# Performance work log

Measured on AMD Instinct MI355X. Metric: run time of the kernel, lower is better.

## Reference

```python
import jax, jax.numpy as jnp
import numpy as np

BATCH, IN_WIDTH, OUT_FEATURES, FAN_IN = 512, 4096, 4096, 128

def setup_inputs() -> dict:
    key = jax.random.key(0)
    k1, k2, k3, k4 = jax.random.split(key, 4)
    input = jax.random.normal(k1, (BATCH, IN_WIDTH), dtype=jnp.float32)
    weight = jax.random.normal(k2, (OUT_FEATURES, FAN_IN), dtype=jnp.float32)
    bias = jax.random.normal(k3, (OUT_FEATURES,), dtype=jnp.float32)
    indx_seqs = jax.random.randint(k4, (OUT_FEATURES, FAN_IN), 0, IN_WIDTH, dtype=jnp.int64)
    return {"input": input, "weight": weight, "bias": bias, "indx_seqs": indx_seqs}

def reference(input, weight, bias, indx_seqs):
    # gather: (B, out_features, fan_in)
    gathered = input[:, indx_seqs]
    # elementwise mul with weight (out_features, fan_in), reduce over fan_in
    return jnp.einsum('bof,of->bo', gathered, weight) + bias
```

## Files before the change

### kernel.cpp

```cpp
#include <hip/hip_runtime.h>
#include <hip/hip_bf16.h>

#define BATCH    512
#define IN_WIDTH 4096
#define OUT_F    4096
#define FAN_IN   128

__global__ __launch_bounds__(256) void k_transpose_in(const float* __restrict__ in,
                                                      __hip_bfloat16* __restrict__ inT) {
  __shared__ float tile[32][33];
  const int jt = blockIdx.x * 32;
  const int bt = blockIdx.y * 32;
  const int tx = threadIdx.x;
  const int ty = threadIdx.y;
#pragma unroll
  for (int r = 0; r < 32; r += 8) {
    tile[ty + r][tx] = in[(size_t)(bt + ty + r) * IN_WIDTH + (jt + tx)];
  }
  __syncthreads();
#pragma unroll
  for (int r = 0; r < 32; r += 8) {
    inT[(size_t)(jt + ty + r) * BATCH + (bt + tx)] = __float2bfloat16(tile[tx][ty + r]);
  }
}

__global__ __launch_bounds__(256) void k_gather_fma(const __hip_bfloat16* __restrict__ inT,
                                                    const float* __restrict__ weight,
                                                    const float* __restrict__ bias,
                                                    const int* __restrict__ idx,
                                                    float* __restrict__ outT) {
  const int o = blockIdx.x;
  const int t = threadIdx.x;
  const int* __restrict__ idxo = idx + (size_t)o * FAN_IN;
  const float* __restrict__ wo = weight + (size_t)o * FAN_IN;
  const uint16_t* __restrict__ inTu = reinterpret_cast<const uint16_t*>(inT);

  float acc0 = 0.f, acc1 = 0.f;
#pragma unroll 8
  for (int f = 0; f < FAN_IN; ++f) {
    const int   j = idxo[f];
    const float w = wo[f];
    const uint32_t v = *reinterpret_cast<const uint32_t*>(inTu + (size_t)j * BATCH + 2 * t);
    const float lo = __uint_as_float(v << 16);
    const float hi = __uint_as_float(v & 0xffff0000u);
    acc0 = fmaf(lo, w, acc0);
    acc1 = fmaf(hi, w, acc1);
  }
  const float bz = bias[o];
  float2 r = make_float2(acc0 + bz, acc1 + bz);
  *reinterpret_cast<float2*>(outT + (size_t)o * BATCH + 2 * t) = r;
}

__global__ __launch_bounds__(256) void k_transpose_out(const float* __restrict__ outT,
                                                       float* __restrict__ out) {
  __shared__ float tile[32][33];
  const int ot = blockIdx.x * 32;
  const int bt = blockIdx.y * 32;
  const int tx = threadIdx.x;
  const int ty = threadIdx.y;
#pragma unroll
  for (int r = 0; r < 32; r += 8) {
    tile[ty + r][tx] = outT[(size_t)(ot + ty + r) * BATCH + (bt + tx)];
  }
  __syncthreads();
#pragma unroll
  for (int r = 0; r < 32; r += 8) {
    out[(size_t)(bt + ty + r) * OUT_F + (ot + tx)] = tile[tx][ty + r];
  }
}

extern "C" void kernel_launch(void* const* d_in, const int* in_sizes, int n_in,
                              void* d_out, int out_size, void* d_ws, size_t ws_size,
                              hipStream_t stream) {
  const float* input  = (const float*)d_in[0];
  const float* weight = (const float*)d_in[1];
  const float* bias   = (const float*)d_in[2];
  const int*   idx    = (const int*)d_in[3];
  float* out = (float*)d_out;

  __hip_bfloat16* inT = (__hip_bfloat16*)d_ws;
  float* outT = (float*)((char*)d_ws + (size_t)IN_WIDTH * BATCH * sizeof(__hip_bfloat16));

  dim3 tblk(32, 8);
  k_transpose_in<<<dim3(IN_WIDTH / 32, BATCH / 32), tblk, 0, stream>>>(input, inT);
  k_gather_fma<<<dim3(OUT_F), dim3(256), 0, stream>>>(inT, weight, bias, idx, outT);
  k_transpose_out<<<dim3(OUT_F / 32, BATCH / 32), tblk, 0, stream>>>(outT, out);
}
```

Baseline: 43.21 us.

## Split transposed input into batch halves and map one wave per output feature

The transposed bf16 input is stored as two batch halves of 256 columns each. The gather kernel now assigns one 64-lane wave per output feature and handles one batch half per block-y, with each lane loading 8 bytes (4 bf16 values) instead of 4. Because the feature index is wave-uniform, the idx and weight loads can become scalar loads, and each gathered row is a 512-byte contiguous chunk. The cost is that the index and weight rows are read twice, once per half, and each wave carries more accumulators.

```diff
diff --git a/kernel.cpp b/kernel.cpp
--- a/kernel.cpp
+++ b/kernel.cpp
@@ -5,9 +5,10 @@
 #define IN_WIDTH 4096
 #define OUT_F    4096
 #define FAN_IN   128
+#define HALF_B   256
 
 __global__ __launch_bounds__(256) void k_transpose_in(const float* __restrict__ in,
-                                                      __hip_bfloat16* __restrict__ inT) {
+                                                      uint16_t* __restrict__ inT) {
   __shared__ float tile[32][33];
   const int jt = blockIdx.x * 32;
   const int bt = blockIdx.y * 32;
@@ -20,35 +21,42 @@
   __syncthreads();
 #pragma unroll
   for (int r = 0; r < 32; r += 8) {
-    inT[(size_t)(jt + ty + r) * BATCH + (bt + tx)] = __float2bfloat16(tile[tx][ty + r]);
+    const int b = bt + tx;
+    const int j = jt + ty + r;
+    __hip_bfloat16 hv = __float2bfloat16(tile[tx][ty + r]);
+    inT[((size_t)(b >> 8) * IN_WIDTH + j) * HALF_B + (b & 255)] =
+        *reinterpret_cast<const uint16_t*>(&hv);
   }
 }
 
-__global__ __launch_bounds__(256) void k_gather_fma(const __hip_bfloat16* __restrict__ inT,
+__global__ __launch_bounds__(256) void k_gather_fma(const uint16_t* __restrict__ inT,
                                                     const float* __restrict__ weight,
                                                     const float* __restrict__ bias,
                                                     const int* __restrict__ idx,
                                                     float* __restrict__ outT) {
-  const int o = blockIdx.x;
-  const int t = threadIdx.x;
-  const int* __restrict__ idxo = idx + (size_t)o * FAN_IN;
-  const float* __restrict__ wo = weight + (size_t)o * FAN_IN;
-  const uint16_t* __restrict__ inTu = reinterpret_cast<const uint16_t*>(inT);
+  const int wave = threadIdx.x >> 6;
+  const int lane = threadIdx.x & 63;
+  const int o = __builtin_amdgcn_readfirstlane(blockIdx.x * 4 + wave);
+  const int h = blockIdx.y;
 
-  float acc0 = 0.f, acc1 = 0.f;
+  const int*   __restrict__ idxo = idx + (size_t)o * FAN_IN;
+  const float* __restrict__ wo   = weight + (size_t)o * FAN_IN;
+  const uint16_t* __restrict__ base = inT + (size_t)h * IN_WIDTH * HALF_B + 4 * lane;
+
+  float a0 = 0.f, a1 = 0.f, a2 = 0.f, a3 = 0.f;
 #pragma unroll 8
   for (int f = 0; f < FAN_IN; ++f) {
     const int   j = idxo[f];
     const float w = wo[f];
-    const uint32_t v = *reinterpret_cast<const uint32_t*>(inTu + (size_t)j * BATCH + 2 * t);
-    const float lo = __uint_as_float(v << 16);
-    const float hi = __uint_as_float(v & 0xffff0000u);
-    acc0 = fmaf(lo, w, acc0);
-    acc1 = fmaf(hi, w, acc1);
+    const uint2 v = *reinterpret_cast<const uint2*>(base + (size_t)j * HALF_B);
+    a0 = fmaf(__uint_as_float(v.x << 16), w, a0);
+    a1 = fmaf(__uint_as_float(v.x & 0xffff0000u), w, a1);
+    a2 = fmaf(__uint_as_float(v.y << 16), w, a2);
+    a3 = fmaf(__uint_as_float(v.y & 0xffff0000u), w, a3);
   }
   const float bz = bias[o];
-  float2 r = make_float2(acc0 + bz, acc1 + bz);
-  *reinterpret_cast<float2*>(outT + (size_t)o * BATCH + 2 * t) = r;
+  float4 r = make_float4(a0 + bz, a1 + bz, a2 + bz, a3 + bz);
+  *reinterpret_cast<float4*>(outT + (size_t)o * BATCH + h * HALF_B + 4 * lane) = r;
 }
 
 __global__ __launch_bounds__(256) void k_transpose_out(const float* __restrict__ outT,
@@ -78,11 +86,11 @@
   const int*   idx    = (const int*)d_in[3];
   float* out = (float*)d_out;
 
-  __hip_bfloat16* inT = (__hip_bfloat16*)d_ws;
-  float* outT = (float*)((char*)d_ws + (size_t)IN_WIDTH * BATCH * sizeof(__hip_bfloat16));
+  uint16_t* inT = (uint16_t*)d_ws;
+  float* outT = (float*)((char*)d_ws + (size_t)IN_WIDTH * BATCH * sizeof(uint16_t));
 
   dim3 tblk(32, 8);
   k_transpose_in<<<dim3(IN_WIDTH / 32, BATCH / 32), tblk, 0, stream>>>(input, inT);
-  k_gather_fma<<<dim3(OUT_F), dim3(256), 0, stream>>>(inT, weight, bias, idx, outT);
+  k_gather_fma<<<dim3(OUT_F / 4, 2), dim3(256), 0, stream>>>(inT, weight, bias, idx, outT);
   k_transpose_out<<<dim3(OUT_F / 32, BATCH / 32), tblk, 0, stream>>>(outT, out);
 }
```

Result: slower. 46.42 us (+7.4%).
